# Optimization experiments

Hardware: AMD Instinct MI355X
Metric: run time of the kernel (lower is better)

The kernel has to match this reference:

```python
import jax, jax.numpy as jnp
import numpy as np

BS, N, IN_F, OUT_F, HEADS = 32, 512, 256, 128, 4
NEG_SLOPE = 0.2


def setup_inputs() -> dict:
    key = jax.random.key(0)
    k1, k2, k3, k4, k5 = jax.random.split(key, 5)
    inputs = jax.random.normal(k1, (BS, N, IN_F), dtype=jnp.float32)
    adj = (jax.random.uniform(k2, (BS, N, N)) > 0.5).astype(jnp.float32)
    # xavier_normal-style init with relu gain sqrt(2)
    w = jax.random.normal(k3, (IN_F, HEADS * OUT_F), dtype=jnp.float32) * (
        np.sqrt(2.0) * np.sqrt(2.0 / (IN_F + HEADS * OUT_F))
    )
    a_i = jax.random.normal(k4, (HEADS, OUT_F, 1), dtype=jnp.float32) * (
        np.sqrt(2.0) * np.sqrt(2.0 / (OUT_F + 1))
    )
    a_j = jax.random.normal(k5, (HEADS, OUT_F, 1), dtype=jnp.float32) * (
        np.sqrt(2.0) * np.sqrt(2.0 / (OUT_F + 1))
    )
    bias = jnp.zeros((HEADS * OUT_F,), dtype=jnp.float32)
    return {"inputs": inputs, "adj": adj, "w": w, "a_i": a_i, "a_j": a_j, "bias": bias}


def reference(inputs, adj, w, a_i, a_j, bias):
    bs, n, _ = inputs.shape
    H, D = a_i.shape[0], a_i.shape[1]
    # self_loop_type == 2: adjacency unchanged
    # project: [bs, n, H, D]
    h = jnp.matmul(inputs, w).reshape(bs, n, H, D)
    # additive attention coefficients: [bs, n, H]
    coeff_i = jnp.einsum('bnhd,hdo->bnho', h, a_i)[..., 0]
    coeff_j = jnp.einsum('bnhd,hdo->bnho', h, a_j)[..., 0]
    # broadcast-sum scores e[b, i, j, h], leaky relu
    e = jax.nn.leaky_relu(coeff_i[:, :, None, :] + coeff_j[:, None, :, :],
                          negative_slope=NEG_SLOPE)
    adj_h = adj[..., None]  # [bs, n, n, 1], broadcasts over heads
    masked_e = jnp.where(adj_h <= 0, jnp.float32(-1e9), e)
    # softmax over neighbor axis j (dim 2), then re-mask
    attention = jax.nn.softmax(masked_e, axis=2) * adj_h
    # dropout = 0.0 -> no-op; normalize=False, average=False
    # per-head aggregation, all heads at once: out[b,i,h,d] = sum_j att[b,i,j,h] h[b,j,h,d]
    out = jnp.einsum('bijh,bjhd->bihd', attention, h).reshape(bs, n, H * D)
    return out + bias
```

## Files before the change

### kernel.cpp

```cpp
#include <hip/hip_runtime.h>

#define BSZ 32
#define NN 512
#define INF 256
#define NH 4
#define HD 512
#define NEG_SLOPE 0.2f

typedef __attribute__((ext_vector_type(8))) short bf16x8;
typedef __attribute__((ext_vector_type(8))) unsigned short ushort8;
typedef __attribute__((ext_vector_type(4))) float f32x4;

static __device__ __forceinline__ unsigned short f2bf(float f) {
    unsigned u = __builtin_bit_cast(unsigned, f);
    return (unsigned short)((u + 0x7FFFu + ((u >> 16) & 1u)) >> 16);
}

static __device__ __forceinline__ bf16x8 pk8(float4 a, float4 b) {
    unsigned d0, d1, d2, d3;
    asm("v_cvt_pk_bf16_f32 %0, %1, %2" : "=v"(d0) : "v"(a.x), "v"(a.y));
    asm("v_cvt_pk_bf16_f32 %0, %1, %2" : "=v"(d1) : "v"(a.z), "v"(a.w));
    asm("v_cvt_pk_bf16_f32 %0, %1, %2" : "=v"(d2) : "v"(b.x), "v"(b.y));
    asm("v_cvt_pk_bf16_f32 %0, %1, %2" : "=v"(d3) : "v"(b.z), "v"(b.w));
    uint4 u; u.x = d0; u.y = d1; u.z = d2; u.w = d3;
    return __builtin_bit_cast(bf16x8, u);
}

static __device__ __forceinline__ void gl_lds16(const void* g, void* l) {
    __builtin_amdgcn_global_load_lds(
        (const __attribute__((address_space(1))) unsigned int*)g,
        (__attribute__((address_space(3))) unsigned int*)l, 16, 0, 0);
}

__global__ __launch_bounds__(256) void kpack_w(const float* __restrict__ w,
                                               unsigned short* __restrict__ wB) {
    int gid = blockIdx.x * 256 + threadIdx.x;
    int c = gid & 511, k = gid >> 9;
    int kb = k >> 5, g = (k >> 3) & 3, e = k & 7;
    wB[(((size_t)(kb * 4 + g) * 512) + c) * 8 + e] = f2bf(w[(size_t)k * 512 + c]);
}

__global__ __launch_bounds__(256) void kmask(const float* __restrict__ adj,
                                             unsigned* __restrict__ mb) {
    const int lane = threadIdx.x & 63, wave = threadIdx.x >> 6;
    const int row0 = blockIdx.x * 8 + wave * 2;
    #pragma unroll
    for (int rr = 0; rr < 2; ++rr) {
        const float* arow = adj + (size_t)(row0 + rr) * NN;
        #pragma unroll
        for (int t = 0; t < 8; ++t) {
            unsigned long long msk = __ballot(arow[t * 64 + lane] > 0.f);
            if (lane == 0) {
                mb[(size_t)(row0 + rr) * 16 + 2 * t]     = (unsigned)msk;
                mb[(size_t)(row0 + rr) * 16 + 2 * t + 1] = (unsigned)(msk >> 32);
            }
        }
    }
}

__global__ __launch_bounds__(256) void k_proj(
    const float* __restrict__ x, const unsigned short* __restrict__ wB,
    const float* __restrict__ ai, const float* __restrict__ aj,
    unsigned short* __restrict__ hB, float* __restrict__ ciT, float* __restrict__ cjT)
{
    __shared__ unsigned short hs[NH * 2048];
    const int tid = threadIdx.x;
    const int lane = tid & 63, head = tid >> 6;
    const int l15 = lane & 15, g = lane >> 4;
    const int row0 = blockIdx.x * 16;

    f32x4 acc[8] = {};
    const float* xp = x + (size_t)(row0 + l15) * INF + g * 8;
    const unsigned short* bp = wB + ((size_t)g * 512 + head * 128 + l15) * 8;

    #pragma unroll
    for (int kb = 0; kb < 8; ++kb) {
        float4 f0 = *(const float4*)(xp + kb * 32);
        float4 f1 = *(const float4*)(xp + kb * 32 + 4);
        bf16x8 a0 = pk8(f0, f1);
        #pragma unroll
        for (int nf = 0; nf < 8; ++nf) {
            bf16x8 bv = *(const bf16x8*)(bp + (size_t)kb * 16384 + nf * 128);
            acc[nf] = __builtin_amdgcn_mfma_f32_16x16x32_bf16(a0, bv, acc[nf], 0, 0, 0);
        }
    }

    float aiv[8], ajv[8];
    #pragma unroll
    for (int nf = 0; nf < 8; ++nf) {
        aiv[nf] = ai[head * 128 + nf * 16 + l15];
        ajv[nf] = aj[head * 128 + nf * 16 + l15];
    }
    const int b = row0 >> 9;
    const int nloc0 = row0 & 511;
    const int kb2 = nloc0 >> 5;
    const int g2base = (nloc0 >> 3) & 3;

    {
        float pi[4] = {0,0,0,0}, pj[4] = {0,0,0,0};
        #pragma unroll
        for (int nf = 0; nf < 8; ++nf)
            #pragma unroll
            for (int reg = 0; reg < 4; ++reg) {
                pi[reg] = fmaf(acc[nf][reg], aiv[nf], pi[reg]);
                pj[reg] = fmaf(acc[nf][reg], ajv[nf], pj[reg]);
            }
        #pragma unroll
        for (int reg = 0; reg < 4; ++reg) {
            #pragma unroll
            for (int off = 1; off < 16; off <<= 1) {
                pi[reg] += __shfl_xor(pi[reg], off);
                pj[reg] += __shfl_xor(pj[reg], off);
            }
        }
        if (l15 == 0) {
            #pragma unroll
            for (int reg = 0; reg < 4; ++reg) {
                int n = nloc0 + 4 * g + reg;
                ciT[((size_t)(head * BSZ + b) * NN) + n] = pi[reg];
                cjT[((size_t)(head * BSZ + b) * NN) + n] = pj[reg];
            }
        }
        #pragma unroll
        for (int reg = 0; reg < 4; ++reg) {
            int jloc = 4 * g + reg;
            int g2l = jloc >> 3, e = jloc & 7;
            #pragma unroll
            for (int nf = 0; nf < 8; ++nf)
                hs[head * 2048 + nf * 256 + g2l * 128 + l15 * 8 + e] =
                    f2bf(acc[nf][reg]);
        }
    }
    __syncthreads();
    {
        ushort8* dst = (ushort8*)(hB + (((size_t)(b * 4 + head) * 16 + kb2) * 4096));
        const ushort8* src = (const ushort8*)(hs + head * 2048);
        #pragma unroll
        for (int it = 0; it < 4; ++it) {
            int u = it * 64 + lane;
            int nf = u >> 5, wdx = u & 31;
            dst[nf * 64 + g2base * 16 + wdx] = src[u];
        }
    }
}

__global__ __launch_bounds__(256, 4) void k_attn(
    const unsigned short* __restrict__ hB, const float* __restrict__ ciT,
    const float* __restrict__ cjT, const unsigned* __restrict__ mb,
    const float* __restrict__ bias, float* __restrict__ out)
{
    __shared__ __align__(16) unsigned short Bst[2][4096];
    __shared__ __align__(16) float cjh[NN];
    __shared__ float cih[64];
    __shared__ unsigned maskS[64][17];
    __shared__ float Mpart[4];

    const int tid = threadIdx.x;
    const int lane = tid & 63, wave = tid >> 6;
    const int l15 = lane & 15, g = lane >> 4;

    const int orig = blockIdx.x;
    const int swz = (orig & 7) * 128 + (orig >> 3);
    const int b  = swz >> 5;
    const int h  = (swz >> 3) & 3;
    const int i0 = (swz & 7) * 64;

    const char* gslab = (const char*)(hB + (size_t)(b * NH + h) * 65536);

    gl_lds16(gslab + wave * 2048 + lane * 16,        (char*)&Bst[0][0] + wave * 2048);
    gl_lds16(gslab + wave * 2048 + 1024 + lane * 16, (char*)&Bst[0][0] + wave * 2048 + 1024);

    {
        const float* src = cjT + (size_t)(h * BSZ + b) * NN;
        float v0 = src[tid], v1 = src[tid + 256];
        cjh[tid] = v0; cjh[tid + 256] = v1;
        float mv = fmaxf(v0, v1);
        #pragma unroll
        for (int off = 32; off; off >>= 1) mv = fmaxf(mv, __shfl_xor(mv, off));
        if (lane == 0) Mpart[wave] = mv;
        if (tid < 64) cih[tid] = ciT[(size_t)(h * BSZ + b) * NN + i0 + tid];
        uint4 m4 = ((const uint4*)(mb + ((size_t)b * NN + i0) * 16))[tid];
        int base = tid * 4, row = base >> 4, wi = base & 15;
        maskS[row][wi] = m4.x; maskS[row][wi + 1] = m4.y;
        maskS[row][wi + 2] = m4.z; maskS[row][wi + 3] = m4.w;
    }
    __syncthreads();

    const float M = fmaxf(fmaxf(Mpart[0], Mpart[1]), fmaxf(Mpart[2], Mpart[3]));
    const float bc = cih[wave * 16 + l15];
    float smx = bc + M;
    const float mrow = fmaxf(smx, NEG_SLOPE * smx);

    float bvv[8];
    #pragma unroll
    for (int nf = 0; nf < 8; ++nf) bvv[nf] = bias[h * 128 + nf * 16 + l15];

    bf16x8 ones;
    #pragma unroll
    for (int e = 0; e < 8; ++e) ones[e] = (short)0x3F80;

    f32x4 acc[8] = {};
    f32x4 accs = {};
    int cur = 0;
    const unsigned* mrowp = maskS[wave * 16 + l15];

    for (int kb = 0; kb < 16; ++kb) {
        if (kb < 15) {
            const char* gs = gslab + (size_t)(kb + 1) * 8192 + wave * 2048 + lane * 16;
            char* ld = (char*)&Bst[cur ^ 1][0] + wave * 2048;
            gl_lds16(gs, ld);
            gl_lds16(gs + 1024, ld + 1024);
        }

        float4 cva = *(const float4*)&cjh[kb * 32 + g * 8];
        float4 cvb = *(const float4*)&cjh[kb * 32 + g * 8 + 4];
        float cj8[8] = {cva.x, cva.y, cva.z, cva.w, cvb.x, cvb.y, cvb.z, cvb.w};
        unsigned byte = (mrowp[kb] >> (g * 8)) & 0xFFu;
        float p[8];
        #pragma unroll
        for (int e = 0; e < 8; ++e) {
            float s = bc + cj8[e];
            s = fmaxf(s, NEG_SLOPE * s);
            float pe = __expf(s - mrow);
            p[e] = ((byte >> e) & 1u) ? pe : 0.f;
        }
        unsigned d0, d1, d2, d3;
        asm("v_cvt_pk_bf16_f32 %0, %1, %2" : "=v"(d0) : "v"(p[0]), "v"(p[1]));
        asm("v_cvt_pk_bf16_f32 %0, %1, %2" : "=v"(d1) : "v"(p[2]), "v"(p[3]));
        asm("v_cvt_pk_bf16_f32 %0, %1, %2" : "=v"(d2) : "v"(p[4]), "v"(p[5]));
        asm("v_cvt_pk_bf16_f32 %0, %1, %2" : "=v"(d3) : "v"(p[6]), "v"(p[7]));
        uint4 u; u.x = d0; u.y = d1; u.z = d2; u.w = d3;
        bf16x8 av = __builtin_bit_cast(bf16x8, u);

        const char* bb = (const char*)&Bst[cur][0] + lane * 16;
        bf16x8 bfr[8];
        #pragma unroll
        for (int nf = 0; nf < 8; ++nf)
            bfr[nf] = *(const bf16x8*)(bb + nf * 1024);

        #pragma unroll
        for (int nf = 0; nf < 8; ++nf)
            acc[nf] = __builtin_amdgcn_mfma_f32_16x16x32_bf16(av, bfr[nf], acc[nf], 0, 0, 0);
        accs = __builtin_amdgcn_mfma_f32_16x16x32_bf16(av, ones, accs, 0, 0, 0);

        if (kb < 15) { __syncthreads(); cur ^= 1; }
    }

    #pragma unroll
    for (int reg = 0; reg < 4; ++reg) {
        float sum = accs[reg];
        float inv = sum > 0.f ? 1.f / sum : 0.f;
        const int i = i0 + wave * 16 + g * 4 + reg;
        #pragma unroll
        for (int nf = 0; nf < 8; ++nf) {
            int colg = h * 128 + nf * 16 + l15;
            out[(size_t)(b * NN + i) * HD + colg] = acc[nf][reg] * inv + bvv[nf];
        }
    }
}

extern "C" void kernel_launch(void* const* d_in, const int* in_sizes, int n_in,
                              void* d_out, int out_size, void* d_ws, size_t ws_size,
                              hipStream_t stream)
{
    const float* x    = (const float*)d_in[0];
    const float* adj  = (const float*)d_in[1];
    const float* w    = (const float*)d_in[2];
    const float* ai   = (const float*)d_in[3];
    const float* aj   = (const float*)d_in[4];
    const float* bias = (const float*)d_in[5];
    float* out = (float*)d_out;

    char* ws = (char*)d_ws;
    unsigned short* wB = (unsigned short*)ws;
    unsigned short* hB = (unsigned short*)(ws + 262144);
    float* ciT         = (float*)(ws + 17039360);
    float* cjT         = (float*)(ws + 17301504);
    unsigned* mb       = (unsigned*)(ws + 17563648);

    kpack_w<<<512, 256, 0, stream>>>(w, wB);
    kmask<<<BSZ * NN / 8, 256, 0, stream>>>(adj, mb);
    k_proj<<<BSZ * NN / 16, 256, 0, stream>>>(x, wB, ai, aj, hB, ciT, cjT);
    k_attn<<<BSZ * NH * (NN / 64), 256, 0, stream>>>(hB, ciT, cjT, mb, bias, out);
}
```

Baseline: 58.03 us.

## Merge weight-pack and mask kernels; double rows per projection block for B reuse

```diff
diff --git a/kernel.cpp b/kernel.cpp
--- a/kernel.cpp
+++ b/kernel.cpp
@@ -32,27 +32,29 @@
         (__attribute__((address_space(3))) unsigned int*)l, 16, 0, 0);
 }
 
-__global__ __launch_bounds__(256) void kpack_w(const float* __restrict__ w,
-                                               unsigned short* __restrict__ wB) {
-    int gid = blockIdx.x * 256 + threadIdx.x;
-    int c = gid & 511, k = gid >> 9;
-    int kb = k >> 5, g = (k >> 3) & 3, e = k & 7;
-    wB[(((size_t)(kb * 4 + g) * 512) + c) * 8 + e] = f2bf(w[(size_t)k * 512 + c]);
-}
-
-__global__ __launch_bounds__(256) void kmask(const float* __restrict__ adj,
-                                             unsigned* __restrict__ mb) {
-    const int lane = threadIdx.x & 63, wave = threadIdx.x >> 6;
-    const int row0 = blockIdx.x * 8 + wave * 2;
-    #pragma unroll
-    for (int rr = 0; rr < 2; ++rr) {
-        const float* arow = adj + (size_t)(row0 + rr) * NN;
-        #pragma unroll
-        for (int t = 0; t < 8; ++t) {
-            unsigned long long msk = __ballot(arow[t * 64 + lane] > 0.f);
-            if (lane == 0) {
-                mb[(size_t)(row0 + rr) * 16 + 2 * t]     = (unsigned)msk;
-                mb[(size_t)(row0 + rr) * 16 + 2 * t + 1] = (unsigned)(msk >> 32);
+__global__ __launch_bounds__(256) void k_prep(
+    const float* __restrict__ w, unsigned short* __restrict__ wB,
+    const float* __restrict__ adj, unsigned* __restrict__ mb)
+{
+    const int bid = blockIdx.x;
+    if (bid < 512) {
+        int gid = bid * 256 + threadIdx.x;
+        int c = gid & 511, k = gid >> 9;
+        int kb = k >> 5, g = (k >> 3) & 3, e = k & 7;
+        wB[(((size_t)(kb * 4 + g) * 512) + c) * 8 + e] = f2bf(w[(size_t)k * 512 + c]);
+    } else {
+        const int lane = threadIdx.x & 63, wave = threadIdx.x >> 6;
+        const int row0 = (bid - 512) * 8 + wave * 2;
+        #pragma unroll
+        for (int rr = 0; rr < 2; ++rr) {
+            const float* arow = adj + (size_t)(row0 + rr) * NN;
+            #pragma unroll
+            for (int t = 0; t < 8; ++t) {
+                unsigned long long msk = __ballot(arow[t * 64 + lane] > 0.f);
+                if (lane == 0) {
+                    mb[(size_t)(row0 + rr) * 16 + 2 * t]     = (unsigned)msk;
+                    mb[(size_t)(row0 + rr) * 16 + 2 * t + 1] = (unsigned)(msk >> 32);
+                }
             }
         }
     }
@@ -63,25 +65,30 @@
     const float* __restrict__ ai, const float* __restrict__ aj,
     unsigned short* __restrict__ hB, float* __restrict__ ciT, float* __restrict__ cjT)
 {
-    __shared__ unsigned short hs[NH * 2048];
+    __shared__ unsigned short hs[NH * 4096];
     const int tid = threadIdx.x;
     const int lane = tid & 63, head = tid >> 6;
     const int l15 = lane & 15, g = lane >> 4;
-    const int row0 = blockIdx.x * 16;
-
-    f32x4 acc[8] = {};
-    const float* xp = x + (size_t)(row0 + l15) * INF + g * 8;
+    const int row0 = blockIdx.x * 32;
+
+    f32x4 acc[2][8] = {};
+    const float* xp0 = x + (size_t)(row0 + l15) * INF + g * 8;
+    const float* xp1 = xp0 + 16 * INF;
     const unsigned short* bp = wB + ((size_t)g * 512 + head * 128 + l15) * 8;
 
     #pragma unroll
     for (int kb = 0; kb < 8; ++kb) {
-        float4 f0 = *(const float4*)(xp + kb * 32);
-        float4 f1 = *(const float4*)(xp + kb * 32 + 4);
+        float4 f0 = *(const float4*)(xp0 + kb * 32);
+        float4 f1 = *(const float4*)(xp0 + kb * 32 + 4);
+        float4 f2 = *(const float4*)(xp1 + kb * 32);
+        float4 f3 = *(const float4*)(xp1 + kb * 32 + 4);
         bf16x8 a0 = pk8(f0, f1);
+        bf16x8 a1 = pk8(f2, f3);
         #pragma unroll
         for (int nf = 0; nf < 8; ++nf) {
             bf16x8 bv = *(const bf16x8*)(bp + (size_t)kb * 16384 + nf * 128);
-            acc[nf] = __builtin_amdgcn_mfma_f32_16x16x32_bf16(a0, bv, acc[nf], 0, 0, 0);
+            acc[0][nf] = __builtin_amdgcn_mfma_f32_16x16x32_bf16(a0, bv, acc[0][nf], 0, 0, 0);
+            acc[1][nf] = __builtin_amdgcn_mfma_f32_16x16x32_bf16(a1, bv, acc[1][nf], 0, 0, 0);
         }
     }
 
@@ -94,16 +101,16 @@
     const int b = row0 >> 9;
     const int nloc0 = row0 & 511;
     const int kb2 = nloc0 >> 5;
-    const int g2base = (nloc0 >> 3) & 3;
-
-    {
+
+    #pragma unroll
+    for (int m = 0; m < 2; ++m) {
         float pi[4] = {0,0,0,0}, pj[4] = {0,0,0,0};
         #pragma unroll
         for (int nf = 0; nf < 8; ++nf)
             #pragma unroll
             for (int reg = 0; reg < 4; ++reg) {
-                pi[reg] = fmaf(acc[nf][reg], aiv[nf], pi[reg]);
-                pj[reg] = fmaf(acc[nf][reg], ajv[nf], pj[reg]);
+                pi[reg] = fmaf(acc[m][nf][reg], aiv[nf], pi[reg]);
+                pj[reg] = fmaf(acc[m][nf][reg], ajv[nf], pj[reg]);
             }
         #pragma unroll
         for (int reg = 0; reg < 4; ++reg) {
@@ -116,31 +123,28 @@
         if (l15 == 0) {
             #pragma unroll
             for (int reg = 0; reg < 4; ++reg) {
-                int n = nloc0 + 4 * g + reg;
+                int n = nloc0 + 16 * m + 4 * g + reg;
                 ciT[((size_t)(head * BSZ + b) * NN) + n] = pi[reg];
                 cjT[((size_t)(head * BSZ + b) * NN) + n] = pj[reg];
             }
         }
         #pragma unroll
         for (int reg = 0; reg < 4; ++reg) {
-            int jloc = 4 * g + reg;
-            int g2l = jloc >> 3, e = jloc & 7;
+            int jloc = 16 * m + 4 * g + reg;
+            int g2 = jloc >> 3, e = jloc & 7;
             #pragma unroll
             for (int nf = 0; nf < 8; ++nf)
-                hs[head * 2048 + nf * 256 + g2l * 128 + l15 * 8 + e] =
-                    f2bf(acc[nf][reg]);
+                hs[head * 4096 + nf * 512 + g2 * 128 + l15 * 8 + e] =
+                    f2bf(acc[m][nf][reg]);
         }
     }
     __syncthreads();
     {
         ushort8* dst = (ushort8*)(hB + (((size_t)(b * 4 + head) * 16 + kb2) * 4096));
-        const ushort8* src = (const ushort8*)(hs + head * 2048);
-        #pragma unroll
-        for (int it = 0; it < 4; ++it) {
-            int u = it * 64 + lane;
-            int nf = u >> 5, wdx = u & 31;
-            dst[nf * 64 + g2base * 16 + wdx] = src[u];
-        }
+        const ushort8* src = (const ushort8*)(hs + head * 4096);
+        #pragma unroll
+        for (int it = 0; it < 8; ++it)
+            dst[it * 64 + lane] = src[it * 64 + lane];
     }
 }
 
@@ -278,8 +282,7 @@
     float* cjT         = (float*)(ws + 17301504);
     unsigned* mb       = (unsigned*)(ws + 17563648);
 
-    kpack_w<<<512, 256, 0, stream>>>(w, wB);
-    kmask<<<BSZ * NN / 8, 256, 0, stream>>>(adj, mb);
-    k_proj<<<BSZ * NN / 16, 256, 0, stream>>>(x, wB, ai, aj, hB, ciT, cjT);
+    k_prep<<<2560, 256, 0, stream>>>(w, wB, adj, mb);
+    k_proj<<<BSZ * NN / 32, 256, 0, stream>>>(x, wB, ai, aj, hB, ciT, cjT);
     k_attn<<<BSZ * NH * (NN / 64), 256, 0, stream>>>(hB, ciT, cjT, mb, bias, out);
 }
```

New measurement: 52.00 us. 10.4% less time.
